# Kernel optimization log

Hardware: AMD Instinct MI355X
Metric: run time of the kernel (lower is better)

The kernel has to match this reference:

```python
import jax, jax.numpy as jnp
import numpy as np

B, S, D = 2, 2048, 1024
H, DK, DV = 16, 64, 64


def setup_inputs() -> dict:
    key = jax.random.key(0)
    ks = jax.random.split(key, 11)
    s = 1.0 / np.sqrt(D)
    inp = {
        "Q": jax.random.normal(ks[0], (B, S, D), jnp.float32),
        "K": jax.random.normal(ks[1], (B, S, D), jnp.float32),
        "V": jax.random.normal(ks[2], (B, S, D), jnp.float32),
        "Wq": jax.random.normal(ks[3], (H, D, DK), jnp.float32) * s,
        "bq": jax.random.normal(ks[4], (H, DK), jnp.float32) * 0.01,
        "Wk": jax.random.normal(ks[5], (H, D, DK), jnp.float32) * s,
        "bk": jax.random.normal(ks[6], (H, DK), jnp.float32) * 0.01,
        "Wv": jax.random.normal(ks[7], (H, D, DV), jnp.float32) * s,
        "bv": jax.random.normal(ks[8], (H, DV), jnp.float32) * 0.01,
        "Wm": jax.random.normal(ks[9], (H * DV, D), jnp.float32) * (1.0 / np.sqrt(H * DV)),
        "bm": jax.random.normal(ks[10], (D,), jnp.float32) * 0.01,
    }
    return inp


def reference(Q, K, V, Wq, bq, Wk, bk, Wv, bv, Wm, bm):
    # Per-head projections (batched over heads instead of a Python loop)
    q = jnp.einsum("bqd,hdk->bhqk", Q, Wq) + bq[None, :, None, :]   # [B,H,S,DK]
    k = jnp.einsum("bsd,hdk->bhsk", K, Wk) + bk[None, :, None, :]   # [B,H,S,DK]
    v = jnp.einsum("bsd,hdv->bhsv", V, Wv) + bv[None, :, None, :]   # [B,H,S,DV]
    scores = jnp.einsum("bhqk,bhsk->bhqs", q, k) / jnp.sqrt(jnp.asarray(DK, q.dtype))
    attn = jax.nn.softmax(scores, axis=-1)                           # [B,H,S,S]
    ctx = jnp.einsum("bhqs,bhsv->bhqv", attn, v)                     # [B,H,S,DV]
    # Concat heads along feature dim, then output projection
    stacked_ctx = jnp.transpose(ctx, (0, 2, 1, 3)).reshape(B, S, H * DV)
    multi_head = stacked_ctx @ Wm + bm                               # [B,S,D]
    # torch.cat(attn_weights_list, dim=-1): [B, S, H*S]
    stacked_attention_weights = jnp.transpose(attn, (0, 2, 1, 3)).reshape(B, S, H * S)
    return multi_head, stacked_attention_weights
```

## Files before the change

### kernel.cpp

```cpp
#include <hip/hip_runtime.h>

#define B_ 2
#define S_ 2048
#define D_ 1024
#define H_ 16
#define M_ 4096

typedef unsigned short u16;
typedef unsigned int u32;
typedef short bf8 __attribute__((ext_vector_type(8)));
typedef float f4 __attribute__((ext_vector_type(4)));

#define MFMA16(a, b, c) __builtin_amdgcn_mfma_f32_16x16x32_bf16(a, b, c, 0, 0, 0)

__device__ __forceinline__ u16 f2b(float f) {
  u32 u = __builtin_bit_cast(u32, f);
  u += 0x7fffu + ((u >> 16) & 1);
  return (u16)(u >> 16);
}
__device__ __forceinline__ u32 pack2(float lo, float hi) {
  return (u32)f2b(lo) | ((u32)f2b(hi) << 16);
}
__device__ __forceinline__ float b2f(u16 h) {
  return __builtin_bit_cast(float, (u32)h << 16);
}
__device__ __forceinline__ bf8 g16(const u16* p) { return *(const bf8*)p; }

__device__ __forceinline__ bf8 ldA(const u16* lds, int rowBase, int kc, int lane) {
  int row = rowBase + (lane & 15);
  int c = (kc * 4 + (lane >> 4)) ^ (row & 7);
  return *(const bf8*)(lds + row * 64 + c * 8);
}

__device__ __forceinline__ void stage_async(u16* ldsdst, const u16* __restrict__ gsrc,
                                            int srcStride, int lane) {
  int row = lane >> 3;
  int c16 = (lane & 7) ^ (row & 7);
  const u16* g = gsrc + (size_t)row * srcStride + c16 * 8;
  __builtin_amdgcn_global_load_lds((const __attribute__((address_space(1))) void*)g,
                                   (__attribute__((address_space(3))) void*)ldsdst,
                                   16, 0, 0);
}

#define WAITVM(N)                                          \
  asm volatile("s_waitcnt vmcnt(" #N ")" ::: "memory");    \
  __builtin_amdgcn_sched_barrier(0)
#define BAR()                      \
  __builtin_amdgcn_s_barrier();    \
  __builtin_amdgcn_sched_barrier(0)

__global__ __launch_bounds__(256) void cvtk3(const float* __restrict__ Q,
                                             const float* __restrict__ K,
                                             const float* __restrict__ V,
                                             u16* __restrict__ Xq,
                                             u16* __restrict__ Xk,
                                             u16* __restrict__ Xv) {
  int z = blockIdx.z;
  const float* in = z == 0 ? Q : z == 1 ? K : V;
  u16* out = z == 0 ? Xq : z == 1 ? Xk : Xv;
  int i = (blockIdx.x * 256 + threadIdx.x) * 8;
  float4 a = *(const float4*)(in + i);
  float4 b = *(const float4*)(in + i + 4);
  uint4 o;
  o.x = pack2(a.x, a.y);
  o.y = pack2(a.z, a.w);
  o.z = pack2(b.x, b.y);
  o.w = pack2(b.z, b.w);
  *(uint4*)(out + i) = o;
}

__global__ __launch_bounds__(256) void tcvt(const float* __restrict__ in,
                                            u16* __restrict__ out, int R, int C) {
  int rt = blockIdx.x, ct = blockIdx.y, z = blockIdx.z;
  in += (size_t)z * R * C;
  out += (size_t)z * R * C;
  __shared__ float tile[64][65];
  int t = threadIdx.x;
  int r = t >> 2, cc = (t & 3) * 16;
#pragma unroll
  for (int j = 0; j < 16; j += 4) {
    float4 v = *(const float4*)(in + (size_t)(rt * 64 + r) * C + ct * 64 + cc + j);
    tile[r][cc + j] = v.x;
    tile[r][cc + j + 1] = v.y;
    tile[r][cc + j + 2] = v.z;
    tile[r][cc + j + 3] = v.w;
  }
  __syncthreads();
  int c = t >> 2;
  u32 buf[8];
#pragma unroll
  for (int j = 0; j < 8; ++j)
    buf[j] = pack2(tile[cc + 2 * j][c], tile[cc + 2 * j + 1][c]);
  uint4* dst = (uint4*)(out + (size_t)(ct * 64 + c) * R + rt * 64 + cc);
  dst[0] = make_uint4(buf[0], buf[1], buf[2], buf[3]);
  dst[1] = make_uint4(buf[4], buf[5], buf[6], buf[7]);
}

__global__ __launch_bounds__(256) void tcvt3(const float* __restrict__ Wq,
                                             const float* __restrict__ Wk,
                                             const float* __restrict__ Wv,
                                             u16* __restrict__ WT0,
                                             u16* __restrict__ WT1,
                                             u16* __restrict__ WT2) {
  int rt = blockIdx.x, z = blockIdx.z;
  int mat = z >> 4, hh = z & 15;
  const float* in = (mat == 0 ? Wq : mat == 1 ? Wk : Wv) + (size_t)hh * 1024 * 64;
  u16* out = (mat == 0 ? WT0 : mat == 1 ? WT1 : WT2) + (size_t)hh * 1024 * 64;
  __shared__ float tile[64][65];
  int t = threadIdx.x;
  int r = t >> 2, cc = (t & 3) * 16;
#pragma unroll
  for (int j = 0; j < 16; j += 4) {
    float4 v = *(const float4*)(in + (size_t)(rt * 64 + r) * 64 + cc + j);
    tile[r][cc + j] = v.x;
    tile[r][cc + j + 1] = v.y;
    tile[r][cc + j + 2] = v.z;
    tile[r][cc + j + 3] = v.w;
  }
  __syncthreads();
  int c = t >> 2;
  u32 buf[8];
#pragma unroll
  for (int j = 0; j < 8; ++j)
    buf[j] = pack2(tile[cc + 2 * j][c], tile[cc + 2 * j + 1][c]);
  uint4* dst = (uint4*)(out + (size_t)c * 1024 + rt * 64 + cc);
  dst[0] = make_uint4(buf[0], buf[1], buf[2], buf[3]);
  dst[1] = make_uint4(buf[4], buf[5], buf[6], buf[7]);
}

__global__ __launch_bounds__(256) void proj4(
    const u16* __restrict__ Xq, const u16* __restrict__ Xk,
    const u16* __restrict__ Xv, const u16* __restrict__ WT0,
    const u16* __restrict__ WT1, const u16* __restrict__ WT2,
    const float* __restrict__ bq, const float* __restrict__ bk,
    const float* __restrict__ bv, u16* __restrict__ qp, u16* __restrict__ kp,
    u16* __restrict__ vTp) {
  int mt = blockIdx.x, nt = blockIdx.y, z = blockIdx.z;
  const u16* Ap = z == 0 ? Xq : z == 1 ? Xk : Xv;
  const u16* BT = z == 0 ? WT0 : z == 1 ? WT1 : WT2;
  const float* bias = z == 0 ? bq : z == 1 ? bk : bv;
  float scale = z == 0 ? 0.125f : 1.0f;
  int t = threadIdx.x, lane = t & 63, w = t >> 6;
  int wr = w >> 1, wc = w & 1;
  int quad = lane >> 4, col = lane & 15;
  __shared__ u16 Asm[2][128 * 64], Bsm[2][128 * 64];

#define PSTG(bi, kt)                                                            \
  {                                                                             \
    _Pragma("unroll") for (int cc_ = 0; cc_ < 4; ++cc_) {                       \
      int rb_ = w * 32 + cc_ * 8;                                               \
      stage_async(Asm[bi] + rb_ * 64,                                           \
                  Ap + (size_t)(mt * 128 + rb_) * 1024 + (kt) * 64, 1024, lane);\
      stage_async(Bsm[bi] + rb_ * 64,                                           \
                  BT + (size_t)(nt * 128 + rb_) * 1024 + (kt) * 64, 1024, lane);\
    }                                                                           \
  }

  f4 acc[4][4] = {};
  PSTG(0, 0);
  WAITVM(0);
  BAR();
  for (int kt = 0; kt < 16; ++kt) {
    int bi = kt & 1;
    if (kt < 15) PSTG(bi ^ 1, kt + 1);
#pragma unroll
    for (int kc = 0; kc < 2; ++kc) {
      bf8 a[4], b[4];
#pragma unroll
      for (int fr = 0; fr < 4; ++fr) a[fr] = ldA(Asm[bi], wr * 64 + fr * 16, kc, lane);
#pragma unroll
      for (int nf = 0; nf < 4; ++nf) b[nf] = ldA(Bsm[bi], wc * 64 + nf * 16, kc, lane);
#pragma unroll
      for (int fr = 0; fr < 4; ++fr)
#pragma unroll
        for (int nf = 0; nf < 4; ++nf)
          acc[fr][nf] = MFMA16(a[fr], b[nf], acc[fr][nf]);
    }
    if (kt < 15) {
      WAITVM(0);
      BAR();
    }
  }
#undef PSTG
  if (z < 2) {
    u16* outp = z == 0 ? qp : kp;
#pragma unroll
    for (int fr = 0; fr < 4; ++fr)
#pragma unroll
      for (int nf = 0; nf < 4; ++nf) {
        int n = nt * 128 + wc * 64 + nf * 16 + col;
        int h = n >> 6, d = n & 63;
        float bs = bias[n];
#pragma unroll
        for (int r = 0; r < 4; ++r) {
          int gm = mt * 128 + wr * 64 + fr * 16 + quad * 4 + r;
          int bb = gm >> 11, s = gm & 2047;
          outp[(size_t)((bb * H_ + h) * S_ + s) * 64 + d] =
              f2b((acc[fr][nf][r] + bs) * scale);
        }
      }
  } else {
#pragma unroll
    for (int fr = 0; fr < 4; ++fr)
#pragma unroll
      for (int nf = 0; nf < 4; ++nf) {
        int n = nt * 128 + wc * 64 + nf * 16 + col;
        int h = n >> 6, d = n & 63;
        float bs = bias[n];
        int s0 = mt * 128 + wr * 64 + fr * 16 + quad * 4;
        int bb = s0 >> 11, s = s0 & 2047;
        uint2 u;
        u.x = pack2(acc[fr][nf][0] + bs, acc[fr][nf][1] + bs);
        u.y = pack2(acc[fr][nf][2] + bs, acc[fr][nf][3] + bs);
        *(uint2*)(vTp + (size_t)((bb * H_ + h) * 64 + d) * S_ + s) = u;
      }
  }
}

__global__ __launch_bounds__(256) void gemmo2(const u16* __restrict__ A,
                                              const u16* __restrict__ BT,
                                              const float* __restrict__ bias,
                                              float* __restrict__ outp) {
  int mt = blockIdx.x, nt = blockIdx.y;
  int t = threadIdx.x, lane = t & 63, w = t >> 6;
  int wr = w >> 1, wc = w & 1;
  int quad = lane >> 4, col = lane & 15;
  __shared__ u16 Asm[2][128 * 64], Bsm[2][128 * 64];

#define PSTG(bi, kt)                                                            \
  {                                                                             \
    _Pragma("unroll") for (int cc_ = 0; cc_ < 4; ++cc_) {                       \
      int rb_ = w * 32 + cc_ * 8;                                               \
      stage_async(Asm[bi] + rb_ * 64,                                           \
                  A + (size_t)(mt * 128 + rb_) * 1024 + (kt) * 64, 1024, lane); \
      stage_async(Bsm[bi] + rb_ * 64,                                           \
                  BT + (size_t)(nt * 128 + rb_) * 1024 + (kt) * 64, 1024, lane);\
    }                                                                           \
  }

  f4 acc[4][4] = {};
  PSTG(0, 0);
  WAITVM(0);
  BAR();
  for (int kt = 0; kt < 16; ++kt) {
    int bi = kt & 1;
    if (kt < 15) PSTG(bi ^ 1, kt + 1);
#pragma unroll
    for (int kc = 0; kc < 2; ++kc) {
      bf8 a[4], b[4];
#pragma unroll
      for (int fr = 0; fr < 4; ++fr) a[fr] = ldA(Asm[bi], wr * 64 + fr * 16, kc, lane);
#pragma unroll
      for (int nf = 0; nf < 4; ++nf) b[nf] = ldA(Bsm[bi], wc * 64 + nf * 16, kc, lane);
#pragma unroll
      for (int fr = 0; fr < 4; ++fr)
#pragma unroll
        for (int nf = 0; nf < 4; ++nf)
          acc[fr][nf] = MFMA16(a[fr], b[nf], acc[fr][nf]);
    }
    if (kt < 15) {
      WAITVM(0);
      BAR();
    }
  }
#undef PSTG
#pragma unroll
  for (int fr = 0; fr < 4; ++fr)
#pragma unroll
    for (int nf = 0; nf < 4; ++nf) {
      int n = nt * 128 + wc * 64 + nf * 16 + col;
      float bs = bias[n];
#pragma unroll
      for (int r = 0; r < 4; ++r) {
        int gm = mt * 128 + wr * 64 + fr * 16 + quad * 4 + r;
        outp[(size_t)gm * 1024 + n] = acc[fr][nf][r] + bs;
      }
    }
}

__global__ void attn7(const u16* __restrict__ qp, const u16* __restrict__ kp,
                      const u16* __restrict__ vT, u16* __restrict__ ctxo,
                      float* __restrict__ attw) {
  int bid = blockIdx.x;
  int l = (bid & 7) * 128 + (bid >> 3);
  int qt = l & 31, hb = l >> 5;
  int h = hb & 15, b = hb >> 4;
  int t = threadIdx.x, lane = t & 63, w = t >> 6;
  int quad = lane >> 4, col = lane & 15;

  __shared__ u16 KV[4][64 * 64];
  __shared__ u16 Psm[4][16 * 64];

  const u16* kbase = kp + (size_t)(b * H_ + h) * S_ * 64;
  const u16* vbase = vT + (size_t)(b * H_ + h) * 64 * S_;
  const u16* qrow = qp + ((size_t)(b * H_ + h) * S_ + qt * 64 + w * 16) * 64;
  int r16 = (lane & 15) * 64;
  int c0 = (lane >> 4) * 8, c1 = c0 + 32;
  bf8 qf0 = g16(qrow + r16 + c0);
  bf8 qf1 = g16(qrow + r16 + c1);

#define SLOT(i) (KV[0] + (size_t)((i) & 3) * 4096)
#define SGT(slot, kt)                                                             \
  {                                                                               \
    u16* s_ = (slot);                                                             \
    const u16* g_ = kbase + (size_t)((kt) & 31) * 4096;                           \
    stage_async(s_ + w * 1024, g_ + w * 16 * 64, 64, lane);                       \
    stage_async(s_ + w * 1024 + 512, g_ + (w * 16 + 8) * 64, 64, lane);           \
  }
#define SGV(bi, kt)                                                               \
  {                                                                               \
    u16* s_ = KV[2 + (bi)];                                                       \
    stage_async(s_ + w * 1024, vbase + (size_t)(w * 16) * S_ + (kt) * 64, S_,     \
                lane);                                                            \
    stage_async(s_ + w * 1024 + 512,                                              \
                vbase + (size_t)(w * 16 + 8) * S_ + (kt) * 64, S_, lane);         \
  }

  SGT(SLOT(0), 0);
  SGT(SLOT(1), 1);
  WAITVM(2);
  BAR();
  float lsum = 0.f;
  for (int kt = 0; kt < 32; ++kt) {
    SGT(SLOT(kt + 2), kt + 2);
    WAITVM(4);
    BAR();
    const u16* Kc = SLOT(kt);
    f4 sc[4] = {};
#pragma unroll
    for (int fr = 0; fr < 4; ++fr) {
      bf8 k0 = ldA(Kc, fr * 16, 0, lane);
      bf8 k1 = ldA(Kc, fr * 16, 1, lane);
      sc[fr] = MFMA16(k0, qf0, sc[fr]);
      sc[fr] = MFMA16(k1, qf1, sc[fr]);
    }
    float s = 0.f;
#pragma unroll
    for (int fr = 0; fr < 4; ++fr)
#pragma unroll
      for (int r = 0; r < 4; ++r) s += __expf(sc[fr][r]);
    lsum += s;
  }
  lsum += __shfl_xor(lsum, 16);
  lsum += __shfl_xor(lsum, 32);
  float linv = 1.f / lsum;

  BAR();
  SGV(0, 0);
  WAITVM(0);
  BAR();
  f4 ctxa[4] = {};
  u16* Pw = Psm[w];
  size_t awrow = ((size_t)(b * S_ + qt * 64 + w * 16) * H_ + h) * S_;
  for (int kt = 0; kt < 32; ++kt) {
    SGT(SLOT((kt + 1) & 1), kt + 1);
    SGV((kt + 1) & 1, (kt + 1) & 31);
    const u16* Kc = SLOT(kt & 1);
    const u16* Vc = KV[2 + (kt & 1)];
    f4 sc[4] = {};
#pragma unroll
    for (int fr = 0; fr < 4; ++fr) {
      bf8 k0 = ldA(Kc, fr * 16, 0, lane);
      bf8 k1 = ldA(Kc, fr * 16, 1, lane);
      sc[fr] = MFMA16(k0, qf0, sc[fr]);
      sc[fr] = MFMA16(k1, qf1, sc[fr]);
    }
#pragma unroll
    for (int fr = 0; fr < 4; ++fr) {
      float p0 = __expf(sc[fr][0]) * linv;
      float p1 = __expf(sc[fr][1]) * linv;
      float p2 = __expf(sc[fr][2]) * linv;
      float p3 = __expf(sc[fr][3]) * linv;
      int bo = col * 128 + ((fr * 32 + quad * 8) ^ ((col & 7) << 4));
      uint2 u;
      u.x = pack2(p0, p1);
      u.y = pack2(p2, p3);
      *(uint2*)((char*)Pw + bo) = u;
    }
#pragma unroll
    for (int it = 0; it < 2; ++it) {
      int row = (lane >> 3) + 8 * it;
      int cc = lane & 7;
      int bo = row * 128 + ((cc ^ (row & 7)) << 4);
      bf8 pv = *(const bf8*)((const char*)Pw + bo);
      float* dst = attw + awrow + (size_t)row * (H_ * S_) + kt * 64 + cc * 8;
      float4 o0, o1;
      o0.x = b2f((u16)pv[0]);
      o0.y = b2f((u16)pv[1]);
      o0.z = b2f((u16)pv[2]);
      o0.w = b2f((u16)pv[3]);
      o1.x = b2f((u16)pv[4]);
      o1.y = b2f((u16)pv[5]);
      o1.z = b2f((u16)pv[6]);
      o1.w = b2f((u16)pv[7]);
      *(float4*)dst = o0;
      *((float4*)dst + 1) = o1;
    }
    bf8 pf0 = ldA(Pw, 0, 0, lane);
    bf8 pf1 = ldA(Pw, 0, 1, lane);
#pragma unroll
    for (int fr = 0; fr < 4; ++fr) {
      bf8 v0 = ldA(Vc, fr * 16, 0, lane);
      bf8 v1 = ldA(Vc, fr * 16, 1, lane);
      ctxa[fr] = MFMA16(v0, pf0, ctxa[fr]);
      ctxa[fr] = MFMA16(v1, pf1, ctxa[fr]);
    }
    WAITVM(4);
    BAR();
  }
  int qg = qt * 64 + w * 16 + col;
  size_t cb = ((size_t)(b * S_ + qg) * H_ + h) * 64;
#pragma unroll
  for (int fr = 0; fr < 4; ++fr) {
    uint2 u;
    u.x = pack2(ctxa[fr][0], ctxa[fr][1]);
    u.y = pack2(ctxa[fr][2], ctxa[fr][3]);
    *(uint2*)(ctxo + cb + fr * 16 + quad * 4) = u;
  }
#undef SLOT
#undef SGT
#undef SGV
}

extern "C" void kernel_launch(void* const* d_in, const int* in_sizes, int n_in,
                              void* d_out, int out_size, void* d_ws, size_t ws_size,
                              hipStream_t stream) {
  const float* Q = (const float*)d_in[0];
  const float* K = (const float*)d_in[1];
  const float* V = (const float*)d_in[2];
  const float* Wq = (const float*)d_in[3];
  const float* bq = (const float*)d_in[4];
  const float* Wk = (const float*)d_in[5];
  const float* bk = (const float*)d_in[6];
  const float* Wv = (const float*)d_in[7];
  const float* bv = (const float*)d_in[8];
  const float* Wm = (const float*)d_in[9];
  const float* bm = (const float*)d_in[10];
  float* out0 = (float*)d_out;
  float* out1 = out0 + (size_t)M_ * D_;
  (void)in_sizes; (void)n_in; (void)out_size; (void)ws_size;

  u16* WT0 = (u16*)d_ws;
  u16* WT1 = WT0 + 1048576;
  u16* WT2 = WT1 + 1048576;
  u16* WT3 = WT2 + 1048576;
  u16* qp = WT3 + 1048576;
  u16* kp = qp + 4194304;
  u16* vTp = kp + 4194304;
  u16* ctx = vTp + 4194304;
  u16* Xk = ctx + 4194304;
  u16* Xv = Xk + 4194304;

  cvtk3<<<dim3(2048, 1, 3), 256, 0, stream>>>(Q, K, V, ctx, Xk, Xv);
  tcvt3<<<dim3(16, 1, 48), 256, 0, stream>>>(Wq, Wk, Wv, WT0, WT1, WT2);
  tcvt<<<dim3(16, 16, 1), 256, 0, stream>>>(Wm, WT3, 1024, 1024);
  proj4<<<dim3(32, 8, 3), 256, 0, stream>>>(ctx, Xk, Xv, WT0, WT1, WT2, bq, bk,
                                            bv, qp, kp, vTp);
  attn7<<<1024, 256, 0, stream>>>(qp, kp, vTp, ctx, out1);
  gemmo2<<<dim3(32, 8), 256, 0, stream>>>(ctx, WT3, bm, out0);
}
```

Before: 288.3 us.

## Merge weight transpose kernels, add MFMA priority hints, unroll softmax-sum pass by two

Combines the two weight-transpose launches into a single launch with a 16x16x49 grid, where blocks covering the per-head QKV weights exit early when ct is nonzero. Wraps MFMA sequences in the projection GEMMs and the attention kernel with s_setprio raises so matrix work gets issue priority. In the attention row-sum pass, two K tiles are staged and processed per barrier instead of one, which halves the barriers. The merged grid launches many empty blocks, and the deeper staging may need more slots than before, so the SLOT indexing must cover four tiles.

Result: slower. 314.6 us (+9.1%).

```diff
diff --git a/kernel.cpp b/kernel.cpp
--- a/kernel.cpp
+++ b/kernel.cpp
@@ -69,11 +69,31 @@
   *(uint4*)(out + i) = o;
 }
 
-__global__ __launch_bounds__(256) void tcvt(const float* __restrict__ in,
-                                            u16* __restrict__ out, int R, int C) {
+__global__ __launch_bounds__(256) void tcvtW(const float* __restrict__ Wq,
+                                             const float* __restrict__ Wk,
+                                             const float* __restrict__ Wv,
+                                             const float* __restrict__ Wm,
+                                             u16* __restrict__ WT0,
+                                             u16* __restrict__ WT1,
+                                             u16* __restrict__ WT2,
+                                             u16* __restrict__ WT3) {
   int rt = blockIdx.x, ct = blockIdx.y, z = blockIdx.z;
-  in += (size_t)z * R * C;
-  out += (size_t)z * R * C;
+  const float* in;
+  u16* out;
+  int R, C;
+  if (z < 48) {
+    if (ct != 0) return;
+    int mat = z >> 4, hh = z & 15;
+    in = (mat == 0 ? Wq : mat == 1 ? Wk : Wv) + (size_t)hh * 1024 * 64;
+    out = (mat == 0 ? WT0 : mat == 1 ? WT1 : WT2) + (size_t)hh * 1024 * 64;
+    R = 1024;
+    C = 64;
+  } else {
+    in = Wm;
+    out = WT3;
+    R = 1024;
+    C = 1024;
+  }
   __shared__ float tile[64][65];
   int t = threadIdx.x;
   int r = t >> 2, cc = (t & 3) * 16;
@@ -92,38 +112,6 @@
   for (int j = 0; j < 8; ++j)
     buf[j] = pack2(tile[cc + 2 * j][c], tile[cc + 2 * j + 1][c]);
   uint4* dst = (uint4*)(out + (size_t)(ct * 64 + c) * R + rt * 64 + cc);
-  dst[0] = make_uint4(buf[0], buf[1], buf[2], buf[3]);
-  dst[1] = make_uint4(buf[4], buf[5], buf[6], buf[7]);
-}
-
-__global__ __launch_bounds__(256) void tcvt3(const float* __restrict__ Wq,
-                                             const float* __restrict__ Wk,
-                                             const float* __restrict__ Wv,
-                                             u16* __restrict__ WT0,
-                                             u16* __restrict__ WT1,
-                                             u16* __restrict__ WT2) {
-  int rt = blockIdx.x, z = blockIdx.z;
-  int mat = z >> 4, hh = z & 15;
-  const float* in = (mat == 0 ? Wq : mat == 1 ? Wk : Wv) + (size_t)hh * 1024 * 64;
-  u16* out = (mat == 0 ? WT0 : mat == 1 ? WT1 : WT2) + (size_t)hh * 1024 * 64;
-  __shared__ float tile[64][65];
-  int t = threadIdx.x;
-  int r = t >> 2, cc = (t & 3) * 16;
-#pragma unroll
-  for (int j = 0; j < 16; j += 4) {
-    float4 v = *(const float4*)(in + (size_t)(rt * 64 + r) * 64 + cc + j);
-    tile[r][cc + j] = v.x;
-    tile[r][cc + j + 1] = v.y;
-    tile[r][cc + j + 2] = v.z;
-    tile[r][cc + j + 3] = v.w;
-  }
-  __syncthreads();
-  int c = t >> 2;
-  u32 buf[8];
-#pragma unroll
-  for (int j = 0; j < 8; ++j)
-    buf[j] = pack2(tile[cc + 2 * j][c], tile[cc + 2 * j + 1][c]);
-  uint4* dst = (uint4*)(out + (size_t)c * 1024 + rt * 64 + cc);
   dst[0] = make_uint4(buf[0], buf[1], buf[2], buf[3]);
   dst[1] = make_uint4(buf[4], buf[5], buf[6], buf[7]);
 }
@@ -170,11 +158,13 @@
       for (int fr = 0; fr < 4; ++fr) a[fr] = ldA(Asm[bi], wr * 64 + fr * 16, kc, lane);
 #pragma unroll
       for (int nf = 0; nf < 4; ++nf) b[nf] = ldA(Bsm[bi], wc * 64 + nf * 16, kc, lane);
+      __builtin_amdgcn_s_setprio(1);
 #pragma unroll
       for (int fr = 0; fr < 4; ++fr)
 #pragma unroll
         for (int nf = 0; nf < 4; ++nf)
           acc[fr][nf] = MFMA16(a[fr], b[nf], acc[fr][nf]);
+      __builtin_amdgcn_s_setprio(0);
     }
     if (kt < 15) {
       WAITVM(0);
@@ -252,11 +242,13 @@
       for (int fr = 0; fr < 4; ++fr) a[fr] = ldA(Asm[bi], wr * 64 + fr * 16, kc, lane);
 #pragma unroll
       for (int nf = 0; nf < 4; ++nf) b[nf] = ldA(Bsm[bi], wc * 64 + nf * 16, kc, lane);
+      __builtin_amdgcn_s_setprio(1);
 #pragma unroll
       for (int fr = 0; fr < 4; ++fr)
 #pragma unroll
         for (int nf = 0; nf < 4; ++nf)
           acc[fr][nf] = MFMA16(a[fr], b[nf], acc[fr][nf]);
+      __builtin_amdgcn_s_setprio(0);
     }
     if (kt < 15) {
       WAITVM(0);
@@ -278,7 +270,7 @@
     }
 }
 
-__global__ void attn7(const u16* __restrict__ qp, const u16* __restrict__ kp,
+__global__ void attn8(const u16* __restrict__ qp, const u16* __restrict__ kp,
                       const u16* __restrict__ vT, u16* __restrict__ ctxo,
                       float* __restrict__ attw) {
   int bid = blockIdx.x;
@@ -315,31 +307,41 @@
     stage_async(s_ + w * 1024 + 512,                                              \
                 vbase + (size_t)(w * 16 + 8) * S_ + (kt) * 64, S_, lane);         \
   }
-
+#define QKT(Kc, sc)                                                               \
+  {                                                                               \
+    _Pragma("unroll") for (int fr = 0; fr < 4; ++fr) {                            \
+      bf8 k0 = ldA(Kc, fr * 16, 0, lane);                                         \
+      bf8 k1 = ldA(Kc, fr * 16, 1, lane);                                         \
+      __builtin_amdgcn_s_setprio(1);                                              \
+      sc[fr] = MFMA16(k0, qf0, sc[fr]);                                           \
+      sc[fr] = MFMA16(k1, qf1, sc[fr]);                                           \
+      __builtin_amdgcn_s_setprio(0);                                              \
+    }                                                                             \
+  }
+
+  float lsum = 0.f;
   SGT(SLOT(0), 0);
   SGT(SLOT(1), 1);
-  WAITVM(2);
+  WAITVM(0);
   BAR();
-  float lsum = 0.f;
-  for (int kt = 0; kt < 32; ++kt) {
+  for (int i = 0; i < 16; ++i) {
+    int kt = 2 * i;
     SGT(SLOT(kt + 2), kt + 2);
+    SGT(SLOT(kt + 3), kt + 3);
     WAITVM(4);
     BAR();
-    const u16* Kc = SLOT(kt);
-    f4 sc[4] = {};
-#pragma unroll
-    for (int fr = 0; fr < 4; ++fr) {
-      bf8 k0 = ldA(Kc, fr * 16, 0, lane);
-      bf8 k1 = ldA(Kc, fr * 16, 1, lane);
-      sc[fr] = MFMA16(k0, qf0, sc[fr]);
-      sc[fr] = MFMA16(k1, qf1, sc[fr]);
-    }
-    float s = 0.f;
-#pragma unroll
-    for (int fr = 0; fr < 4; ++fr)
-#pragma unroll
-      for (int r = 0; r < 4; ++r) s += __expf(sc[fr][r]);
-    lsum += s;
+#pragma unroll
+    for (int half = 0; half < 2; ++half) {
+      const u16* Kc = SLOT(kt + half);
+      f4 sc[4] = {};
+      QKT(Kc, sc);
+      float s = 0.f;
+#pragma unroll
+      for (int fr = 0; fr < 4; ++fr)
+#pragma unroll
+        for (int r = 0; r < 4; ++r) s += __expf(sc[fr][r]);
+      lsum += s;
+    }
   }
   lsum += __shfl_xor(lsum, 16);
   lsum += __shfl_xor(lsum, 32);
@@ -358,13 +360,7 @@
     const u16* Kc = SLOT(kt & 1);
     const u16* Vc = KV[2 + (kt & 1)];
     f4 sc[4] = {};
-#pragma unroll
-    for (int fr = 0; fr < 4; ++fr) {
-      bf8 k0 = ldA(Kc, fr * 16, 0, lane);
-      bf8 k1 = ldA(Kc, fr * 16, 1, lane);
-      sc[fr] = MFMA16(k0, qf0, sc[fr]);
-      sc[fr] = MFMA16(k1, qf1, sc[fr]);
-    }
+    QKT(Kc, sc);
 #pragma unroll
     for (int fr = 0; fr < 4; ++fr) {
       float p0 = __expf(sc[fr][0]) * linv;
@@ -402,8 +398,10 @@
     for (int fr = 0; fr < 4; ++fr) {
       bf8 v0 = ldA(Vc, fr * 16, 0, lane);
       bf8 v1 = ldA(Vc, fr * 16, 1, lane);
+      __builtin_amdgcn_s_setprio(1);
       ctxa[fr] = MFMA16(v0, pf0, ctxa[fr]);
       ctxa[fr] = MFMA16(v1, pf1, ctxa[fr]);
+      __builtin_amdgcn_s_setprio(0);
     }
     WAITVM(4);
     BAR();
@@ -420,6 +418,7 @@
 #undef SLOT
 #undef SGT
 #undef SGV
+#undef QKT
 }
 
 extern "C" void kernel_launch(void* const* d_in, const int* in_sizes, int n_in,
@@ -452,10 +451,9 @@
   u16* Xv = Xk + 4194304;
 
   cvtk3<<<dim3(2048, 1, 3), 256, 0, stream>>>(Q, K, V, ctx, Xk, Xv);
-  tcvt3<<<dim3(16, 1, 48), 256, 0, stream>>>(Wq, Wk, Wv, WT0, WT1, WT2);
-  tcvt<<<dim3(16, 16, 1), 256, 0, stream>>>(Wm, WT3, 1024, 1024);
+  tcvtW<<<dim3(16, 16, 49), 256, 0, stream>>>(Wq, Wk, Wv, Wm, WT0, WT1, WT2, WT3);
   proj4<<<dim3(32, 8, 3), 256, 0, stream>>>(ctx, Xk, Xv, WT0, WT1, WT2, bq, bk,
                                             bv, qp, kp, vTp);
-  attn7<<<1024, 256, 0, stream>>>(qp, kp, vTp, ctx, out1);
+  attn8<<<1024, 256, 0, stream>>>(qp, kp, vTp, ctx, out1);
   gemmo2<<<dim3(32, 8), 256, 0, stream>>>(ctx, WT3, bm, out0);
 }
```
